# Optimization experiments

Measured on AMD Instinct MI355X. Metric: run time of the kernel, lower is better.

Reference implementation:

```python
import jax, jax.numpy as jnp
import numpy as np

DIM = 256      # d_model (MCMoE default dim=256)
E = 4          # experts: [CoAFusion, SNNFusion, DAMISLFusion, DropX2Fusion]
K = 2          # max_experts (top-k in cosine gate)
ATT = 128      # gated-attention hidden dim in DAMISL MIL pooling
N1, N2, B = 16384, 4096, 1


def setup_inputs() -> dict:
    key = jax.random.key(0)
    ks = jax.random.split(key, 16)
    s = 1.0 / np.sqrt(DIM)
    f32 = jnp.float32
    lin = lambda k, shape, scale: jax.random.normal(k, shape, f32) * scale
    return {
        'x1': jax.random.normal(ks[0], (B, N1, DIM), f32),
        'x2': jax.random.normal(ks[1], (B, N2, DIM), f32),
        # MM_CosineGate params: per-expert prototype rows + activation thresholds
        'sim_matrix': lin(ks[2], (E, DIM), 1.0),
        'gates': jnp.zeros((E,), f32),
        # SNNFusion: RMSNorm scales + two SNN blocks (Linear+ELU)
        'g1': jnp.ones((DIM,), f32),
        'g2': jnp.ones((DIM,), f32),
        'snn_w1': lin(ks[3], (DIM, DIM), s), 'snn_b1': jnp.zeros((DIM,), f32),
        'snn_w2': lin(ks[4], (DIM, DIM), s), 'snn_b2': jnp.zeros((DIM,), f32),
        # CoAFusion: single-head cross attention x1 -> x2
        'wq': lin(ks[5], (DIM, DIM), s), 'wk': lin(ks[6], (DIM, DIM), s),
        'wv': lin(ks[7], (DIM, DIM), s), 'wo': lin(ks[8], (DIM, DIM), s),
        # DAMISLFusion: gated-attention MIL pooling over x2 + fuse linear
        'va': lin(ks[9], (DIM, ATT), s), 'ua': lin(ks[10], (DIM, ATT), s),
        'wa': lin(ks[11], (ATT, 1), 1.0 / np.sqrt(ATT)),
        'wf': lin(ks[12], (DIM, DIM), s),
    }


def _rms(x, g):
    return x * jax.lax.rsqrt(jnp.mean(x * x, axis=-1, keepdims=True) + 1e-6) * g


def _forward(x1, x2, sim_matrix, gates, g1, g2, snn_w1, snn_b1, snn_w2, snn_b2,
             wq, wk, wv, wo, va, ua, wa, wf):
    # ---- MM_CosineGate: cosine similarity of pooled multimodal feature vs prototypes
    f = 0.5 * (x1.mean(axis=1) + x2.mean(axis=1))                       # [B, D]
    fn = f * jax.lax.rsqrt(jnp.sum(f * f, -1, keepdims=True) + 1e-8)
    sn = sim_matrix * jax.lax.rsqrt(jnp.sum(sim_matrix * sim_matrix, -1, keepdims=True) + 1e-8)
    scores = fn @ sn.T                                                  # [B, E]
    topv = jax.lax.top_k(scores, K)[0]                                  # [B, K]
    keep = (scores >= topv[:, -1:]) & (scores > gates[None, :])         # top-k AND above gate
    logits = jnp.where(keep, scores, 0.0)                               # [B, E], 0 for inactive

    # ---- Expert 0: CoAFusion (cross attention, residual)
    attn = jax.nn.softmax(
        jnp.einsum('bnd,bmd->bnm', x1 @ wq, x2 @ wk) / np.sqrt(DIM), axis=-1)  # [B, N1, N2]
    e0 = x1 + jnp.einsum('bnm,bmd->bnd', attn, x2 @ wv) @ wo

    # ---- Expert 1: SNNFusion (per-token SNN on x1 + pooled SNN on x2)
    e1 = jax.nn.elu(_rms(x1, g1) @ snn_w1 + snn_b1) \
         + jax.nn.elu(_rms(x2, g2) @ snn_w2 + snn_b2).mean(axis=1, keepdims=True)

    # ---- Expert 2: DAMISLFusion (gated-attention MIL pool of x2, broadcast fuse)
    h = jnp.tanh(x2 @ va) * jax.nn.sigmoid(x2 @ ua)                     # [B, N2, ATT]
    a = jax.nn.softmax((h @ wa)[..., 0], axis=1)                        # [B, N2]
    pooled = jnp.einsum('bm,bmd->bd', a, x2)                            # [B, D]
    e2 = x1 + (pooled @ wf)[:, None, :]

    # ---- Expert 3: DropX2Fusion (identity on x1)
    e3 = x1

    # ---- Weighted combine over selected experts (weight 0 => expert contributes 0),
    # then divide by number of selected experts (matches `outputs /= num_selected`).
    w = logits
    out = (w[:, 0, None, None] * e0 + w[:, 1, None, None] * e1
           + w[:, 2, None, None] * e2 + w[:, 3, None, None] * e3)
    num_sel = jnp.maximum(jnp.sum(logits > 0, axis=-1), 1).astype(out.dtype)  # [B]
    return out / num_sel[:, None, None]


def reference(x1, x2, sim_matrix, gates, g1, g2, snn_w1, snn_b1, snn_w2, snn_b2,
              wq, wk, wv, wo, va, ua, wa, wf):
    return _forward(x1, x2, sim_matrix, gates, g1, g2, snn_w1, snn_b1,
                    snn_w2, snn_b2, wq, wk, wv, wo, va, ua, wa, wf)
```

## Files before the change

kernel.cpp:

```cpp
#include <hip/hip_runtime.h>
#include <math.h>

#define N1 16384
#define N2 4096
#define DIM 256
#define ATT 128

typedef unsigned int uint32;
typedef __attribute__((ext_vector_type(4))) short s4v;
typedef __attribute__((ext_vector_type(8))) short s8v;
typedef __attribute__((ext_vector_type(16))) float f16v;
typedef __attribute__((ext_vector_type(2))) uint32 u2v;
typedef __attribute__((ext_vector_type(4))) uint32 u4v;

union S8U { s8v v; s4v h[2]; };

#define AS1C const __attribute__((address_space(1)))
#define AS3 __attribute__((address_space(3)))

#define WS_KPK 0
#define WS_VPK 524288
#define WS_WQT 1048576
#define WS_WOT 1081344
#define WS_W1T 1114112
#define WS_WKT 1146880
#define WS_WVT 1179648
#define WS_W2T 1212416
#define WS_VAT 1245184
#define WS_UAT 1261568
#define WS_ACC 1277952
#define WS_COLSUM1 (WS_ACC)
#define WS_COLSUM2 (WS_ACC+256)
#define WS_S2SUM  (WS_ACC+512)
#define WS_POOLED (WS_ACC+768)
#define WS_ALOGIT (WS_ACC+1024)
#define WS_AW     (WS_ALOGIT+4096)
#define WS_CVEC   (WS_AW+4096)
#define WS_GATE   (WS_CVEC+256)

#define L_K    0
#define L_V    65536
#define L_P    131072
#define L_LP   147456
#define L_LINV 149504
#define L_RRS  149760
#define L_RR   150016
#define L_X1PK  0
#define L_QPAD  65536
#define L_OBUF  0
#define L_X1PK2 65536
#define SMEM_BYTES 150272

__device__ __forceinline__ uint32 f2bf1(float f) {
    uint32 u = __float_as_uint(f);
    return (u + 0x7fffu + ((u >> 16) & 1u)) >> 16;
}
__device__ __forceinline__ uint32 f2bf2(float lo, float hi) {
    return f2bf1(lo) | (f2bf1(hi) << 16);
}
#define MFMA32(a, b, c) __builtin_amdgcn_mfma_f32_32x32x16_bf16((a), (b), (c), 0, 0, 0)

__global__ __launch_bounds__(256) void k_colsum12(const float* __restrict__ x1,
                                                  const float* __restrict__ x2,
                                                  float* __restrict__ ws)
{
    const int t = threadIdx.x;
    const int b = blockIdx.x;
    const float* src = (b < 256) ? x1 : x2;
    const int rbase = ((b < 256) ? b : (b - 256)) * 64;
    const int dsti = (b < 256) ? (WS_COLSUM1 + t) : (WS_COLSUM2 + t);
    float acc = 0.f;
    for (int r = 0; r < 64; ++r) acc += src[(size_t)(rbase + r) * DIM + t];
    atomicAdd(&ws[dsti], acc);
}

__global__ __launch_bounds__(256) void k_wpack(const float* __restrict__ wq,
    const float* __restrict__ wo, const float* __restrict__ snn_w1,
    const float* __restrict__ wk, const float* __restrict__ wv,
    const float* __restrict__ snn_w2,
    const float* __restrict__ va, const float* __restrict__ ua,
    const float* __restrict__ g1, const float* __restrict__ g2,
    float* __restrict__ ws)
{
    const int b = blockIdx.x;
    const int t = threadIdx.x;
    int mat, chunk, ncols;
    if (b < 192) { mat = b >> 5; chunk = b & 31; ncols = 256; }
    else { mat = 6 + ((b - 192) >> 4); chunk = (b - 192) & 15; ncols = 128; }
    const float* W;
    int dstoff;
    switch (mat) {
        case 0: W = wq;     dstoff = WS_WQT; break;
        case 1: W = wo;     dstoff = WS_WOT; break;
        case 2: W = snn_w1; dstoff = WS_W1T; break;
        case 3: W = wk;     dstoff = WS_WKT; break;
        case 4: W = wv;     dstoff = WS_WVT; break;
        case 5: W = snn_w2; dstoff = WS_W2T; break;
        case 6: W = va;     dstoff = WS_VAT; break;
        default: W = ua;    dstoff = WS_UAT; break;
    }
    unsigned short* dst = (unsigned short*)(ws + dstoff);
    const int e0 = chunk * 2048 + t * 8;
    const int k = (ncols == 256) ? (e0 >> 8) : (e0 >> 7);
    const int n0 = (ncols == 256) ? (e0 & 255) : (e0 & 127);
    const float4 v0 = *(const float4*)(W + k * ncols + n0);
    const float4 v1 = *(const float4*)(W + k * ncols + n0 + 4);
    const float sc = (mat == 2) ? g1[k] : ((mat == 5) ? g2[k] : 1.0f);
    float vals[8] = {v0.x, v0.y, v0.z, v0.w, v1.x, v1.y, v1.z, v1.w};
    const unsigned int sbase = (unsigned int)(k >> 4) * 512u + 32u * ((k >> 3) & 1) * 8u + (k & 7);
    #pragma unroll
    for (int jj = 0; jj < 8; ++jj) {
        const int n = n0 + jj;
        unsigned int off = (unsigned int)(n >> 5) * 16u * 512u + sbase + (unsigned int)(n & 31) * 8u;
        dst[off] = (unsigned short)f2bf1(vals[jj] * sc);
    }
}

__global__ __launch_bounds__(512) void k_x2prep2(const float* __restrict__ x2,
    const float* __restrict__ b2, const float* __restrict__ wa,
    float* __restrict__ ws)
{
    __shared__ char xps[16384];
    __shared__ float rrs[32];
    __shared__ float dlp[4][32];
    const int t = threadIdx.x;
    const int w = t >> 6;
    const int lane = t & 63;
    const int l31 = lane & 31;
    const int lh = lane >> 5;
    const int b = blockIdx.x;
    const int tb = b * 32;
    unsigned short* kpk = (unsigned short*)(ws + WS_KPK);
    unsigned short* vpk = (unsigned short*)(ws + WS_VPK);
    const char* wsb = (const char*)ws;
    const char* wkt = wsb + (size_t)WS_WKT * 4;
    const char* wvt = wsb + (size_t)WS_WVT * 4;
    const char* w2t = wsb + (size_t)WS_W2T * 4;
    const char* vat = wsb + (size_t)WS_VAT * 4;
    const char* uat = wsb + (size_t)WS_UAT * 4;

    #pragma unroll
    for (int i = 0; i < 2; ++i) {
        const int c = t + 512 * i;
        const int tk = c >> 5, d0 = (c & 31) * 8;
        const float4 a = *(const float4*)(x2 + (size_t)(tb + tk) * DIM + d0);
        const float4 bb = *(const float4*)(x2 + (size_t)(tb + tk) * DIM + d0 + 4);
        float ss = a.x*a.x + a.y*a.y + a.z*a.z + a.w*a.w
                 + bb.x*bb.x + bb.y*bb.y + bb.z*bb.z + bb.w*bb.w;
        #pragma unroll
        for (int o = 16; o > 0; o >>= 1) ss += __shfl_down(ss, o, 32);
        if ((t & 31) == 0) rrs[tk] = ss;
        u4v pk;
        pk.x = f2bf2(a.x, a.y); pk.y = f2bf2(a.z, a.w);
        pk.z = f2bf2(bb.x, bb.y); pk.w = f2bf2(bb.z, bb.w);
        *(u4v*)(xps + (d0 >> 4) * 1024 + (tk + 32 * ((d0 >> 3) & 1)) * 16) = pk;
    }
    __syncthreads();

    {
        f16v kacc = (f16v)0.0f;
        #pragma unroll
        for (int s = 0; s < 16; ++s) {
            const s8v a = *(const s8v*)(wkt + (w * 16 + s) * 1024 + lane * 16);
            const s8v bb = *(const s8v*)(xps + s * 1024 + lane * 16);
            kacc = MFMA32(a, bb, kacc);
        }
        #pragma unroll
        for (int g = 0; g < 4; ++g) {
            const unsigned int chunkK = (unsigned int)((b >> 1) * 32 + 2 * (2 * w + (g >> 1)) + (b & 1));
            const unsigned int off = chunkK * 512u + (unsigned int)(l31 + 32 * (g & 1)) * 8u + 4u * lh;
            u2v pk;
            pk.x = f2bf2(kacc[4 * g + 0], kacc[4 * g + 1]);
            pk.y = f2bf2(kacc[4 * g + 2], kacc[4 * g + 3]);
            *(u2v*)(kpk + off) = pk;
        }
    }
    {
        f16v vacc = (f16v)0.0f;
        #pragma unroll
        for (int s = 0; s < 16; ++s) {
            const s8v a = *(const s8v*)(xps + s * 1024 + lane * 16);
            const s8v bb = *(const s8v*)(wvt + (w * 16 + s) * 1024 + lane * 16);
            vacc = MFMA32(a, bb, vacc);
        }
        #pragma unroll
        for (int g = 0; g < 4; ++g) {
            const unsigned int chunkV = (unsigned int)((b >> 1) * 32 + 4 * w + 2 * (b & 1) + (g >> 1));
            const unsigned int off = chunkV * 512u + (unsigned int)(l31 + 32 * (g & 1)) * 8u + 4u * lh;
            u2v pk;
            pk.x = f2bf2(vacc[4 * g + 0], vacc[4 * g + 1]);
            pk.y = f2bf2(vacc[4 * g + 2], vacc[4 * g + 3]);
            *(u2v*)(vpk + off) = pk;
        }
    }
    {
        f16v sacc = (f16v)0.0f;
        #pragma unroll
        for (int s = 0; s < 16; ++s) {
            const s8v a = *(const s8v*)(w2t + (w * 16 + s) * 1024 + lane * 16);
            const s8v bb = *(const s8v*)(xps + s * 1024 + lane * 16);
            sacc = MFMA32(a, bb, sacc);
        }
        const float rrl = rsqrtf(rrs[l31] * (1.0f / DIM) + 1e-6f);
        #pragma unroll
        for (int g = 0; g < 4; ++g) {
            const float4 bb = *(const float4*)(b2 + 32 * w + 8 * g + 4 * lh);
            #pragma unroll
            for (int jj = 0; jj < 4; ++jj) {
                float v = sacc[4 * g + jj] * rrl + ((const float*)&bb)[jj];
                v = (v > 0.f) ? v : expm1f(v);
                v += __shfl_xor(v, 16); v += __shfl_xor(v, 8);
                v += __shfl_xor(v, 4);  v += __shfl_xor(v, 2);
                v += __shfl_xor(v, 1);
                if (l31 == 0) atomicAdd(&ws[WS_S2SUM + 32 * w + 8 * g + 4 * lh + jj], v);
            }
        }
    }
    if (w < 4) {
        f16v hv = (f16v)0.0f, hu = (f16v)0.0f;
        #pragma unroll
        for (int s = 0; s < 16; ++s) {
            const s8v bb = *(const s8v*)(xps + s * 1024 + lane * 16);
            const s8v a1 = *(const s8v*)(vat + (w * 16 + s) * 1024 + lane * 16);
            const s8v a2 = *(const s8v*)(uat + (w * 16 + s) * 1024 + lane * 16);
            hv = MFMA32(a1, bb, hv);
            hu = MFMA32(a2, bb, hu);
        }
        float acc = 0.f;
        #pragma unroll
        for (int g = 0; g < 4; ++g) {
            const float4 w4 = *(const float4*)(wa + 32 * w + 8 * g + 4 * lh);
            #pragma unroll
            for (int jj = 0; jj < 4; ++jj) {
                acc += tanhf(hv[4 * g + jj]) * (1.0f / (1.0f + expf(-hu[4 * g + jj])))
                       * ((const float*)&w4)[jj];
            }
        }
        acc += __shfl_xor(acc, 32);
        if (lh == 0) dlp[w][l31] = acc;
    }
    __syncthreads();
    if (t < 32) ws[WS_ALOGIT + tb + t] = dlp[0][t] + dlp[1][t] + dlp[2][t] + dlp[3][t];
}

__device__ __forceinline__ float block_sum256(float v, float* red, int t)
{
    red[t] = v; __syncthreads();
    for (int s = 128; s > 0; s >>= 1) { if (t < s) red[t] += red[t + s]; __syncthreads(); }
    const float r = red[0]; __syncthreads(); return r;
}
__device__ __forceinline__ float block_max256(float v, float* red, int t)
{
    red[t] = v; __syncthreads();
    for (int s = 128; s > 0; s >>= 1) { if (t < s) red[t] = fmaxf(red[t], red[t + s]); __syncthreads(); }
    const float r = red[0]; __syncthreads(); return r;
}

__global__ __launch_bounds__(256) void k_gate(const float* __restrict__ sim,
    const float* __restrict__ gates, float* __restrict__ ws)
{
    __shared__ float red[256];
    __shared__ float sc[4];
    const int t = threadIdx.x;
    const float f = 0.5f * (ws[WS_COLSUM1 + t] * (1.0f / N1) +
                            ws[WS_COLSUM2 + t] * (1.0f / N2));
    const float fs = block_sum256(f * f, red, t);
    const float rsqf = rsqrtf(fs + 1e-8f);
    for (int e = 0; e < 4; ++e) {
        const float sv = sim[e * DIM + t];
        const float n2 = block_sum256(sv * sv, red, t);
        const float dt = block_sum256(sv * f, red, t);
        if (t == 0) sc[e] = dt * rsqf * rsqrtf(n2 + 1e-8f);
    }
    __syncthreads();
    if (t == 0) {
        float a = -1e30f, b = -1e30f;
        #pragma unroll
        for (int e = 0; e < 4; ++e) {
            const float v = sc[e];
            if (v > a) { b = a; a = v; } else if (v > b) { b = v; }
        }
        float w[4]; int ns = 0;
        #pragma unroll
        for (int e = 0; e < 4; ++e) {
            const bool keep = (sc[e] >= b) && (sc[e] > gates[e]);
            w[e] = keep ? sc[e] : 0.f;
            if (w[e] > 0.f) ns++;
        }
        if (ns < 1) ns = 1;
        ws[WS_GATE + 0] = w[0]; ws[WS_GATE + 1] = w[1];
        ws[WS_GATE + 2] = w[2]; ws[WS_GATE + 3] = w[3];
        ws[WS_GATE + 4] = 1.0f / (float)ns;
        ws[WS_GATE + 5] = w[0] + w[2] + w[3];
    }
    __syncthreads();
    float mx = -1e30f;
    for (int i = t; i < N2; i += 256) mx = fmaxf(mx, ws[WS_ALOGIT + i]);
    mx = block_max256(mx, red, t);
    float sm = 0.f;
    for (int i = t; i < N2; i += 256) {
        const float e_ = expf(ws[WS_ALOGIT + i] - mx);
        ws[WS_AW + i] = e_;
        sm += e_;
    }
    sm = block_sum256(sm, red, t);
    const float is = 1.0f / sm;
    for (int i = t; i < N2; i += 256) ws[WS_AW + i] *= is;
}

__global__ __launch_bounds__(256) void k_pooled(const float* __restrict__ x2,
                                                float* __restrict__ ws)
{
    const int t = threadIdx.x;
    const int rbase = blockIdx.x * 64;
    float acc = 0.f;
    for (int r = 0; r < 64; ++r)
        acc = fmaf(ws[WS_AW + rbase + r], x2[(size_t)(rbase + r) * DIM + t], acc);
    atomicAdd(&ws[WS_POOLED + t], acc);
}

__global__ __launch_bounds__(256) void k_cvec(const float* __restrict__ wf,
                                              float* __restrict__ ws)
{
    __shared__ float pl[256];
    const int t = threadIdx.x;
    pl[t] = ws[WS_POOLED + t];
    __syncthreads();
    float acc = 0.f;
    for (int k = 0; k < 256; ++k) acc = fmaf(pl[k], wf[k * DIM + t], acc);
    const float w1 = ws[WS_GATE + 1], w2 = ws[WS_GATE + 2];
    ws[WS_CVEC + t] = w1 * (ws[WS_S2SUM + t] * (1.0f / N2)) + w2 * acc;
}

__global__ __launch_bounds__(512, 2) void k_flash(
    const float* __restrict__ x1, const float* __restrict__ b1,
    const float* __restrict__ wsf, float* __restrict__ out)
{
    extern __shared__ char sm[];
    const int t = threadIdx.x;
    const int w = t >> 6;
    const int lane = t & 63;
    const int l31 = lane & 31;
    const int lh = lane >> 5;
    const int qb = blockIdx.x * 64;
    const int kh = w >> 1, qh = w & 1;
    const int qp = w & 1, dpair = w >> 1;
    const char* wsb = (const char*)wsf;
    const char* kpk = wsb + (size_t)WS_KPK * 4;
    const char* vpk = wsb + (size_t)WS_VPK * 4;
    const char* wqt = wsb + (size_t)WS_WQT * 4;
    const char* wot = wsb + (size_t)WS_WOT * 4;
    const char* w1t = wsb + (size_t)WS_W1T * 4;

    auto stage64 = [&](const char* gbase, int ldsoff) {
        #pragma unroll
        for (int i = 0; i < 8; ++i) {
            const int c = w * 8 + i;
            __builtin_amdgcn_global_load_lds(
                (AS1C uint32*)(gbase + c * 1024 + lane * 16),
                (AS3 uint32*)(sm + ldsoff + c * 1024), 16, 0, 0);
        }
    };

    #pragma unroll
    for (int i = 0; i < 4; ++i) {
        const int c = t + 512 * i;
        const int q = c >> 5, d0 = (c & 31) * 8;
        const float4 a = *(const float4*)(x1 + (size_t)(qb + q) * DIM + d0);
        const float4 b = *(const float4*)(x1 + (size_t)(qb + q) * DIM + d0 + 4);
        float ss = a.x*a.x + a.y*a.y + a.z*a.z + a.w*a.w
                 + b.x*b.x + b.y*b.y + b.z*b.z + b.w*b.w;
        #pragma unroll
        for (int o = 16; o > 0; o >>= 1) ss += __shfl_down(ss, o, 32);
        if ((t & 31) == 0) *(float*)(sm + L_RRS + q * 4) = ss;
        u4v pk;
        pk.x = f2bf2(a.x, a.y); pk.y = f2bf2(a.z, a.w);
        pk.z = f2bf2(b.x, b.y); pk.w = f2bf2(b.z, b.w);
        *(u4v*)(sm + L_X1PK + ((q >> 5) * 16 + (d0 >> 4)) * 1024
                + ((q & 31) + 32 * ((d0 >> 3) & 1)) * 16) = pk;
    }
    __syncthreads();
    if (t < 64) {
        const float s2 = *(const float*)(sm + L_RRS + t * 4);
        *(float*)(sm + L_RR + t * 4) = rsqrtf(s2 * (1.0f / DIM) + 1e-6f);
    }
    #pragma unroll
    for (int i = 0; i < 2; ++i) {
        const int mt = w, qt = i;
        f16v qa = (f16v)0.0f;
        #pragma unroll
        for (int s = 0; s < 16; ++s) {
            const s8v a  = *(const s8v*)(wqt + (mt * 16 + s) * 1024 + lane * 16);
            const s8v bb = *(const s8v*)(sm + L_X1PK + (qt * 16 + s) * 1024 + lane * 16);
            qa = MFMA32(a, bb, qa);
        }
        const int q = qt * 32 + l31;
        #pragma unroll
        for (int g = 0; g < 4; ++g) {
            const int d0 = 32 * mt + 8 * g + 4 * lh;
            u2v pk;
            pk.x = f2bf2(qa[4 * g + 0], qa[4 * g + 1]);
            pk.y = f2bf2(qa[4 * g + 2], qa[4 * g + 3]);
            *(u2v*)(sm + L_QPAD + q * 520 + d0 * 2) = pk;
        }
    }
    __syncthreads();
    s8v qf[16];
    {
        const char* qbase = sm + L_QPAD + (qh * 32 + l31) * 520 + lh * 16;
        #pragma unroll
        for (int s = 0; s < 16; ++s) {
            S8U u;
            u.h[0] = *(const s4v*)(qbase + s * 32);
            u.h[1] = *(const s4v*)(qbase + s * 32 + 8);
            qf[s] = u.v;
        }
    }
    stage64(kpk, L_K);
    __syncthreads();

    f16v oacc0a = (f16v)0.0f, oacc0b = (f16v)0.0f;
    f16v oacc1a = (f16v)0.0f, oacc1b = (f16v)0.0f;
    float lsum = 0.0f;

    for (int tile = 0; tile < 32; ++tile) {
        stage64(vpk + (size_t)tile * 65536, L_V);
        f16v sacc0 = (f16v)0.0f, sacc1 = (f16v)0.0f;
        #pragma unroll
        for (int s2 = 0; s2 < 8; ++s2) {
            const s8v a0 = *(const s8v*)(sm + L_K
                + ((kh >> 1) * 32 + 2 * (2 * s2) + (kh & 1)) * 1024 + lane * 16);
            const s8v a1 = *(const s8v*)(sm + L_K
                + ((kh >> 1) * 32 + 2 * (2 * s2 + 1) + (kh & 1)) * 1024 + lane * 16);
            sacc0 = MFMA32(a0, qf[2 * s2], sacc0);
            sacc1 = MFMA32(a1, qf[2 * s2 + 1], sacc1);
        }
        #pragma unroll
        for (int g = 0; g < 4; ++g) {
            const float p0 = __expf((sacc0[4 * g + 0] + sacc1[4 * g + 0]) * 0.0625f);
            const float p1 = __expf((sacc0[4 * g + 1] + sacc1[4 * g + 1]) * 0.0625f);
            const float p2 = __expf((sacc0[4 * g + 2] + sacc1[4 * g + 2]) * 0.0625f);
            const float p3 = __expf((sacc0[4 * g + 3] + sacc1[4 * g + 3]) * 0.0625f);
            lsum += (p0 + p1) + (p2 + p3);
            const int keyo = 32 * kh + 8 * g + 4 * lh;
            const int kc = keyo >> 4, ko = keyo & 15;
            u2v pk; pk.x = f2bf2(p0, p1); pk.y = f2bf2(p2, p3);
            *(u2v*)(sm + L_P + (qh * 8 + kc) * 1024
                    + (l31 + 32 * (ko >> 3)) * 16 + (ko & 7) * 2) = pk;
        }
        __syncthreads();
        if (tile < 31) stage64(kpk + (size_t)(tile + 1) * 65536, L_K);
        s8v pf[8];
        #pragma unroll
        for (int kc = 0; kc < 8; ++kc)
            pf[kc] = *(const s8v*)(sm + L_P + (qp * 8 + kc) * 1024 + lane * 16);
        #pragma unroll
        for (int kc = 0; kc < 4; ++kc) {
            const int sub = 0, k3 = kc;
            const s8v a0 = *(const s8v*)(sm + L_V + (sub + 4 * (2 * dpair) + k3) * 1024 + lane * 16);
            const s8v a1 = *(const s8v*)(sm + L_V + (sub + 4 * (2 * dpair + 1) + k3) * 1024 + lane * 16);
            oacc0a = MFMA32(a0, pf[kc], oacc0a);
            oacc1a = MFMA32(a1, pf[kc], oacc1a);
        }
        #pragma unroll
        for (int kc = 4; kc < 8; ++kc) {
            const int sub = 32, k3 = kc & 3;
            const s8v a0 = *(const s8v*)(sm + L_V + (sub + 4 * (2 * dpair) + k3) * 1024 + lane * 16);
            const s8v a1 = *(const s8v*)(sm + L_V + (sub + 4 * (2 * dpair + 1) + k3) * 1024 + lane * 16);
            oacc0b = MFMA32(a0, pf[kc], oacc0b);
            oacc1b = MFMA32(a1, pf[kc], oacc1b);
        }
        __syncthreads();
    }

    *(float*)(sm + L_LP + ((w * 2 + lh) * 32 + l31) * 4) = lsum;
    __syncthreads();
    if (t < 64) {
        const int qh_ = t >> 5, c = t & 31;
        const float* lp = (const float*)(sm + L_LP);
        float l = 0.f;
        #pragma unroll
        for (int k2 = 0; k2 < 4; ++k2)
            l += lp[((k2 * 2 + qh_) * 2 + 0) * 32 + c]
               + lp[((k2 * 2 + qh_) * 2 + 1) * 32 + c];
        *(float*)(sm + L_LINV + t * 4) = 1.0f / l;
    }
    __syncthreads();
    {
        const float li = *(const float*)(sm + L_LINV + (qp * 32 + l31) * 4);
        #pragma unroll
        for (int half = 0; half < 2; ++half) {
            const f16v accA = half ? oacc1a : oacc0a;
            const f16v accB = half ? oacc1b : oacc0b;
            const int dc = 2 * dpair + half;
            #pragma unroll
            for (int g = 0; g < 4; ++g) {
                const int d0 = dc * 32 + 8 * g + 4 * lh;
                u2v pk;
                pk.x = f2bf2((accA[4 * g + 0] + accB[4 * g + 0]) * li,
                             (accA[4 * g + 1] + accB[4 * g + 1]) * li);
                pk.y = f2bf2((accA[4 * g + 2] + accB[4 * g + 2]) * li,
                             (accA[4 * g + 3] + accB[4 * g + 3]) * li);
                *(u2v*)(sm + L_OBUF + (qp * 16 + (d0 >> 4)) * 1024
                        + (l31 + 32 * ((d0 >> 3) & 1)) * 16 + (d0 & 7) * 2) = pk;
            }
        }
    }
    #pragma unroll
    for (int i = 0; i < 4; ++i) {
        const int c = t + 512 * i;
        const int q = c >> 5, d0 = (c & 31) * 8;
        const float4 a = *(const float4*)(x1 + (size_t)(qb + q) * DIM + d0);
        const float4 b = *(const float4*)(x1 + (size_t)(qb + q) * DIM + d0 + 4);
        u4v pk;
        pk.x = f2bf2(a.x, a.y); pk.y = f2bf2(a.z, a.w);
        pk.z = f2bf2(b.x, b.y); pk.w = f2bf2(b.z, b.w);
        *(u4v*)(sm + L_X1PK2 + ((q >> 5) * 16 + (d0 >> 4)) * 1024
                + ((q & 31) + 32 * ((d0 >> 3) & 1)) * 16) = pk;
    }
    __syncthreads();
    const float gw0 = wsf[WS_GATE + 0], gw1 = wsf[WS_GATE + 1];
    const float ginv = wsf[WS_GATE + 4], gcx1 = wsf[WS_GATE + 5];
    #pragma unroll
    for (int i = 0; i < 2; ++i) {
        const int mt = w, qt = i;
        f16v ea = (f16v)0.0f, sa = (f16v)0.0f;
        for (int s = 0; s < 16; ++s) {
            const s8v awo = *(const s8v*)(wot + (mt * 16 + s) * 1024 + lane * 16);
            const s8v aw1 = *(const s8v*)(w1t + (mt * 16 + s) * 1024 + lane * 16);
            const s8v bo = *(const s8v*)(sm + L_OBUF + (qt * 16 + s) * 1024 + lane * 16);
            const s8v bx = *(const s8v*)(sm + L_X1PK2 + (qt * 16 + s) * 1024 + lane * 16);
            ea = MFMA32(awo, bo, ea);
            sa = MFMA32(aw1, bx, sa);
        }
        const int q = qt * 32 + l31;
        const float rrq = *(const float*)(sm + L_RR + q * 4);
        #pragma unroll
        for (int g = 0; g < 4; ++g) {
            const int d0 = 32 * mt + 8 * g + 4 * lh;
            const float4 cv = *(const float4*)(wsf + WS_CVEC + d0);
            const float4 bb = *(const float4*)(b1 + d0);
            const float4 xx = *(const float4*)(x1 + (size_t)(qb + q) * DIM + d0);
            float ev0 = sa[4 * g + 0] * rrq + bb.x; ev0 = (ev0 > 0.f) ? ev0 : expm1f(ev0);
            float ev1 = sa[4 * g + 1] * rrq + bb.y; ev1 = (ev1 > 0.f) ? ev1 : expm1f(ev1);
            float ev2 = sa[4 * g + 2] * rrq + bb.z; ev2 = (ev2 > 0.f) ? ev2 : expm1f(ev2);
            float ev3 = sa[4 * g + 3] * rrq + bb.w; ev3 = (ev3 > 0.f) ? ev3 : expm1f(ev3);
            float4 o;
            o.x = ginv * (gcx1 * xx.x + gw0 * ea[4 * g + 0] + gw1 * ev0 + cv.x);
            o.y = ginv * (gcx1 * xx.y + gw0 * ea[4 * g + 1] + gw1 * ev1 + cv.y);
            o.z = ginv * (gcx1 * xx.z + gw0 * ea[4 * g + 2] + gw1 * ev2 + cv.z);
            o.w = ginv * (gcx1 * xx.w + gw0 * ea[4 * g + 3] + gw1 * ev3 + cv.w);
            *(float4*)(out + (size_t)(qb + q) * DIM + d0) = o;
        }
    }
}

extern "C" void kernel_launch(void* const* d_in, const int* in_sizes, int n_in,
                              void* d_out, int out_size, void* d_ws, size_t ws_size,
                              hipStream_t stream)
{
    (void)in_sizes; (void)n_in; (void)out_size; (void)ws_size;
    const float* x1    = (const float*)d_in[0];
    const float* x2    = (const float*)d_in[1];
    const float* sim   = (const float*)d_in[2];
    const float* gates = (const float*)d_in[3];
    const float* g1    = (const float*)d_in[4];
    const float* g2    = (const float*)d_in[5];
    const float* w1m   = (const float*)d_in[6];
    const float* b1    = (const float*)d_in[7];
    const float* w2m   = (const float*)d_in[8];
    const float* b2    = (const float*)d_in[9];
    const float* wq    = (const float*)d_in[10];
    const float* wk    = (const float*)d_in[11];
    const float* wv    = (const float*)d_in[12];
    const float* wo    = (const float*)d_in[13];
    const float* va    = (const float*)d_in[14];
    const float* ua    = (const float*)d_in[15];
    const float* wa    = (const float*)d_in[16];
    const float* wf    = (const float*)d_in[17];
    float* ws  = (float*)d_ws;
    float* out = (float*)d_out;

    hipMemsetAsync(ws + WS_ACC, 0, 1024 * sizeof(float), stream);
    hipLaunchKernelGGL(k_colsum12, dim3(320), dim3(256), 0, stream, x1, x2, ws);
    hipLaunchKernelGGL(k_wpack, dim3(224), dim3(256), 0, stream,
                       wq, wo, w1m, wk, wv, w2m, va, ua, g1, g2, ws);
    hipLaunchKernelGGL(k_x2prep2, dim3(N2 / 32), dim3(512), 0, stream, x2, b2, wa, ws);
    hipLaunchKernelGGL(k_gate, dim3(1), dim3(256), 0, stream, sim, gates, ws);
    hipLaunchKernelGGL(k_pooled, dim3(N2 / 64), dim3(256), 0, stream, x2, ws);
    hipLaunchKernelGGL(k_cvec, dim3(1), dim3(256), 0, stream, wf, ws);
    hipLaunchKernelGGL(k_flash, dim3(N1 / 64), dim3(512), SMEM_BYTES, stream,
                       x1, b1, ws, out);
}
```

Baseline: 278.3 us.

## Fuse all stages into one cooperative persistent kernel with grid syncs

```diff
diff --git a/kernel.cpp b/kernel.cpp
--- a/kernel.cpp
+++ b/kernel.cpp
@@ -1,5 +1,8 @@
 #include <hip/hip_runtime.h>
+#include <hip/hip_cooperative_groups.h>
 #include <math.h>
+
+namespace cg = cooperative_groups;
 
 #define N1 16384
 #define N2 4096
@@ -60,497 +63,504 @@
 }
 #define MFMA32(a, b, c) __builtin_amdgcn_mfma_f32_32x32x16_bf16((a), (b), (c), 0, 0, 0)
 
-__global__ __launch_bounds__(256) void k_colsum12(const float* __restrict__ x1,
-                                                  const float* __restrict__ x2,
-                                                  float* __restrict__ ws)
+__global__ __launch_bounds__(512, 2) void k_all(
+    const float* __restrict__ x1, const float* __restrict__ x2,
+    const float* __restrict__ sim, const float* __restrict__ gates,
+    const float* __restrict__ g1, const float* __restrict__ g2,
+    const float* __restrict__ snn_w1, const float* __restrict__ b1,
+    const float* __restrict__ snn_w2, const float* __restrict__ b2,
+    const float* __restrict__ wq, const float* __restrict__ wk,
+    const float* __restrict__ wv, const float* __restrict__ wo,
+    const float* __restrict__ va, const float* __restrict__ ua,
+    const float* __restrict__ wa, const float* __restrict__ wf,
+    float* __restrict__ ws, float* __restrict__ out)
 {
+    extern __shared__ char sm[];
+    cg::grid_group grid = cg::this_grid();
     const int t = threadIdx.x;
     const int b = blockIdx.x;
-    const float* src = (b < 256) ? x1 : x2;
-    const int rbase = ((b < 256) ? b : (b - 256)) * 64;
-    const int dsti = (b < 256) ? (WS_COLSUM1 + t) : (WS_COLSUM2 + t);
-    float acc = 0.f;
-    for (int r = 0; r < 64; ++r) acc += src[(size_t)(rbase + r) * DIM + t];
-    atomicAdd(&ws[dsti], acc);
-}
-
-__global__ __launch_bounds__(256) void k_wpack(const float* __restrict__ wq,
-    const float* __restrict__ wo, const float* __restrict__ snn_w1,
-    const float* __restrict__ wk, const float* __restrict__ wv,
-    const float* __restrict__ snn_w2,
-    const float* __restrict__ va, const float* __restrict__ ua,
-    const float* __restrict__ g1, const float* __restrict__ g2,
-    float* __restrict__ ws)
-{
-    const int b = blockIdx.x;
-    const int t = threadIdx.x;
-    int mat, chunk, ncols;
-    if (b < 192) { mat = b >> 5; chunk = b & 31; ncols = 256; }
-    else { mat = 6 + ((b - 192) >> 4); chunk = (b - 192) & 15; ncols = 128; }
-    const float* W;
-    int dstoff;
-    switch (mat) {
-        case 0: W = wq;     dstoff = WS_WQT; break;
-        case 1: W = wo;     dstoff = WS_WOT; break;
-        case 2: W = snn_w1; dstoff = WS_W1T; break;
-        case 3: W = wk;     dstoff = WS_WKT; break;
-        case 4: W = wv;     dstoff = WS_WVT; break;
-        case 5: W = snn_w2; dstoff = WS_W2T; break;
-        case 6: W = va;     dstoff = WS_VAT; break;
-        default: W = ua;    dstoff = WS_UAT; break;
-    }
-    unsigned short* dst = (unsigned short*)(ws + dstoff);
-    const int e0 = chunk * 2048 + t * 8;
-    const int k = (ncols == 256) ? (e0 >> 8) : (e0 >> 7);
-    const int n0 = (ncols == 256) ? (e0 & 255) : (e0 & 127);
-    const float4 v0 = *(const float4*)(W + k * ncols + n0);
-    const float4 v1 = *(const float4*)(W + k * ncols + n0 + 4);
-    const float sc = (mat == 2) ? g1[k] : ((mat == 5) ? g2[k] : 1.0f);
-    float vals[8] = {v0.x, v0.y, v0.z, v0.w, v1.x, v1.y, v1.z, v1.w};
-    const unsigned int sbase = (unsigned int)(k >> 4) * 512u + 32u * ((k >> 3) & 1) * 8u + (k & 7);
-    #pragma unroll
-    for (int jj = 0; jj < 8; ++jj) {
-        const int n = n0 + jj;
-        unsigned int off = (unsigned int)(n >> 5) * 16u * 512u + sbase + (unsigned int)(n & 31) * 8u;
-        dst[off] = (unsigned short)f2bf1(vals[jj] * sc);
-    }
-}
-
-__global__ __launch_bounds__(512) void k_x2prep2(const float* __restrict__ x2,
-    const float* __restrict__ b2, const float* __restrict__ wa,
-    float* __restrict__ ws)
-{
-    __shared__ char xps[16384];
-    __shared__ float rrs[32];
-    __shared__ float dlp[4][32];
-    const int t = threadIdx.x;
     const int w = t >> 6;
     const int lane = t & 63;
     const int l31 = lane & 31;
     const int lh = lane >> 5;
-    const int b = blockIdx.x;
-    const int tb = b * 32;
-    unsigned short* kpk = (unsigned short*)(ws + WS_KPK);
-    unsigned short* vpk = (unsigned short*)(ws + WS_VPK);
-    const char* wsb = (const char*)ws;
-    const char* wkt = wsb + (size_t)WS_WKT * 4;
-    const char* wvt = wsb + (size_t)WS_WVT * 4;
-    const char* w2t = wsb + (size_t)WS_W2T * 4;
-    const char* vat = wsb + (size_t)WS_VAT * 4;
-    const char* uat = wsb + (size_t)WS_UAT * 4;
-
-    #pragma unroll
-    for (int i = 0; i < 2; ++i) {
-        const int c = t + 512 * i;
-        const int tk = c >> 5, d0 = (c & 31) * 8;
-        const float4 a = *(const float4*)(x2 + (size_t)(tb + tk) * DIM + d0);
-        const float4 bb = *(const float4*)(x2 + (size_t)(tb + tk) * DIM + d0 + 4);
-        float ss = a.x*a.x + a.y*a.y + a.z*a.z + a.w*a.w
-                 + bb.x*bb.x + bb.y*bb.y + bb.z*bb.z + bb.w*bb.w;
+
+    if (b == 0) {
+        for (int i = t; i < 1024; i += 512) ws[WS_ACC + i] = 0.f;
+    }
+    __threadfence();
+    grid.sync();
+
+    if (t < 256) {
+        if (b < 224) {
+            int mat, chunk, ncols;
+            if (b < 192) { mat = b >> 5; chunk = b & 31; ncols = 256; }
+            else { mat = 6 + ((b - 192) >> 4); chunk = (b - 192) & 15; ncols = 128; }
+            const float* W;
+            int dstoff;
+            switch (mat) {
+                case 0: W = wq;     dstoff = WS_WQT; break;
+                case 1: W = wo;     dstoff = WS_WOT; break;
+                case 2: W = snn_w1; dstoff = WS_W1T; break;
+                case 3: W = wk;     dstoff = WS_WKT; break;
+                case 4: W = wv;     dstoff = WS_WVT; break;
+                case 5: W = snn_w2; dstoff = WS_W2T; break;
+                case 6: W = va;     dstoff = WS_VAT; break;
+                default: W = ua;    dstoff = WS_UAT; break;
+            }
+            unsigned short* dst = (unsigned short*)(ws + dstoff);
+            const int e0 = chunk * 2048 + t * 8;
+            const int k = (ncols == 256) ? (e0 >> 8) : (e0 >> 7);
+            const int n0 = (ncols == 256) ? (e0 & 255) : (e0 & 127);
+            const float4 v0 = *(const float4*)(W + k * ncols + n0);
+            const float4 v1 = *(const float4*)(W + k * ncols + n0 + 4);
+            const float sc = (mat == 2) ? g1[k] : ((mat == 5) ? g2[k] : 1.0f);
+            float vals[8] = {v0.x, v0.y, v0.z, v0.w, v1.x, v1.y, v1.z, v1.w};
+            const unsigned int sbase = (unsigned int)(k >> 4) * 512u
+                + 32u * ((k >> 3) & 1) * 8u + (k & 7);
+            #pragma unroll
+            for (int jj = 0; jj < 8; ++jj) {
+                const int n = n0 + jj;
+                unsigned int off = (unsigned int)(n >> 5) * 16u * 512u + sbase
+                                 + (unsigned int)(n & 31) * 8u;
+                dst[off] = (unsigned short)f2bf1(vals[jj] * sc);
+            }
+        }
+    } else {
+        const int col = t - 256;
+        float acc = 0.f;
+        for (int r = 0; r < 64; ++r) acc += x1[(size_t)(b * 64 + r) * DIM + col];
+        atomicAdd(&ws[WS_COLSUM1 + col], acc);
+        if (b < 64) {
+            float a2 = 0.f;
+            for (int r = 0; r < 64; ++r) a2 += x2[(size_t)(b * 64 + r) * DIM + col];
+            atomicAdd(&ws[WS_COLSUM2 + col], a2);
+        }
+    }
+    __threadfence();
+    grid.sync();
+
+    if (b < 128) {
+        char* xps = sm;
+        float* rrs = (float*)(sm + 16384);
+        float* dlp = (float*)(sm + 16512);
+        const int tb = b * 32;
+        unsigned short* kpk = (unsigned short*)(ws + WS_KPK);
+        unsigned short* vpk = (unsigned short*)(ws + WS_VPK);
+        const char* wsb = (const char*)ws;
+        const char* wkt = wsb + (size_t)WS_WKT * 4;
+        const char* wvt = wsb + (size_t)WS_WVT * 4;
+        const char* w2t = wsb + (size_t)WS_W2T * 4;
+        const char* vat = wsb + (size_t)WS_VAT * 4;
+        const char* uat = wsb + (size_t)WS_UAT * 4;
+
         #pragma unroll
-        for (int o = 16; o > 0; o >>= 1) ss += __shfl_down(ss, o, 32);
-        if ((t & 31) == 0) rrs[tk] = ss;
-        u4v pk;
-        pk.x = f2bf2(a.x, a.y); pk.y = f2bf2(a.z, a.w);
-        pk.z = f2bf2(bb.x, bb.y); pk.w = f2bf2(bb.z, bb.w);
-        *(u4v*)(xps + (d0 >> 4) * 1024 + (tk + 32 * ((d0 >> 3) & 1)) * 16) = pk;
+        for (int i = 0; i < 2; ++i) {
+            const int c = t + 512 * i;
+            const int tk = c >> 5, d0 = (c & 31) * 8;
+            const float4 a = *(const float4*)(x2 + (size_t)(tb + tk) * DIM + d0);
+            const float4 bb = *(const float4*)(x2 + (size_t)(tb + tk) * DIM + d0 + 4);
+            float ss = a.x*a.x + a.y*a.y + a.z*a.z + a.w*a.w
+                     + bb.x*bb.x + bb.y*bb.y + bb.z*bb.z + bb.w*bb.w;
+            #pragma unroll
+            for (int o = 16; o > 0; o >>= 1) ss += __shfl_down(ss, o, 32);
+            if ((t & 31) == 0) rrs[tk] = ss;
+            u4v pk;
+            pk.x = f2bf2(a.x, a.y); pk.y = f2bf2(a.z, a.w);
+            pk.z = f2bf2(bb.x, bb.y); pk.w = f2bf2(bb.z, bb.w);
+            *(u4v*)(xps + (d0 >> 4) * 1024 + (tk + 32 * ((d0 >> 3) & 1)) * 16) = pk;
+        }
+        __syncthreads();
+
+        {
+            f16v kacc = (f16v)0.0f;
+            #pragma unroll
+            for (int s = 0; s < 16; ++s) {
+                const s8v a = *(const s8v*)(wkt + (w * 16 + s) * 1024 + lane * 16);
+                const s8v bb = *(const s8v*)(xps + s * 1024 + lane * 16);
+                kacc = MFMA32(a, bb, kacc);
+            }
+            #pragma unroll
+            for (int g = 0; g < 4; ++g) {
+                const unsigned int chunkK =
+                    (unsigned int)((b >> 1) * 32 + 2 * (2 * w + (g >> 1)) + (b & 1));
+                const unsigned int off = chunkK * 512u
+                    + (unsigned int)(l31 + 32 * (g & 1)) * 8u + 4u * lh;
+                u2v pk;
+                pk.x = f2bf2(kacc[4 * g + 0], kacc[4 * g + 1]);
+                pk.y = f2bf2(kacc[4 * g + 2], kacc[4 * g + 3]);
+                *(u2v*)(kpk + off) = pk;
+            }
+        }
+        {
+            f16v vacc = (f16v)0.0f;
+            #pragma unroll
+            for (int s = 0; s < 16; ++s) {
+                const s8v a = *(const s8v*)(xps + s * 1024 + lane * 16);
+                const s8v bb = *(const s8v*)(wvt + (w * 16 + s) * 1024 + lane * 16);
+                vacc = MFMA32(a, bb, vacc);
+            }
+            #pragma unroll
+            for (int g = 0; g < 4; ++g) {
+                const unsigned int chunkV =
+                    (unsigned int)((b >> 1) * 32 + 4 * w + 2 * (b & 1) + (g >> 1));
+                const unsigned int off = chunkV * 512u
+                    + (unsigned int)(l31 + 32 * (g & 1)) * 8u + 4u * lh;
+                u2v pk;
+                pk.x = f2bf2(vacc[4 * g + 0], vacc[4 * g + 1]);
+                pk.y = f2bf2(vacc[4 * g + 2], vacc[4 * g + 3]);
+                *(u2v*)(vpk + off) = pk;
+            }
+        }
+        {
+            f16v sacc = (f16v)0.0f;
+            #pragma unroll
+            for (int s = 0; s < 16; ++s) {
+                const s8v a = *(const s8v*)(w2t + (w * 16 + s) * 1024 + lane * 16);
+                const s8v bb = *(const s8v*)(xps + s * 1024 + lane * 16);
+                sacc = MFMA32(a, bb, sacc);
+            }
+            const float rrl = rsqrtf(rrs[l31] * (1.0f / DIM) + 1e-6f);
+            #pragma unroll
+            for (int g = 0; g < 4; ++g) {
+                const float4 bb = *(const float4*)(b2 + 32 * w + 8 * g + 4 * lh);
+                #pragma unroll
+                for (int jj = 0; jj < 4; ++jj) {
+                    float v = sacc[4 * g + jj] * rrl + ((const float*)&bb)[jj];
+                    v = (v > 0.f) ? v : expm1f(v);
+                    v += __shfl_xor(v, 16); v += __shfl_xor(v, 8);
+                    v += __shfl_xor(v, 4);  v += __shfl_xor(v, 2);
+                    v += __shfl_xor(v, 1);
+                    if (l31 == 0)
+                        atomicAdd(&ws[WS_S2SUM + 32 * w + 8 * g + 4 * lh + jj], v);
+                }
+            }
+        }
+        if (w < 4) {
+            f16v hv = (f16v)0.0f, hu = (f16v)0.0f;
+            #pragma unroll
+            for (int s = 0; s < 16; ++s) {
+                const s8v bb = *(const s8v*)(xps + s * 1024 + lane * 16);
+                const s8v a1 = *(const s8v*)(vat + (w * 16 + s) * 1024 + lane * 16);
+                const s8v a2 = *(const s8v*)(uat + (w * 16 + s) * 1024 + lane * 16);
+                hv = MFMA32(a1, bb, hv);
+                hu = MFMA32(a2, bb, hu);
+            }
+            float acc = 0.f;
+            #pragma unroll
+            for (int g = 0; g < 4; ++g) {
+                const float4 w4 = *(const float4*)(wa + 32 * w + 8 * g + 4 * lh);
+                #pragma unroll
+                for (int jj = 0; jj < 4; ++jj) {
+                    acc += tanhf(hv[4 * g + jj])
+                         * (1.0f / (1.0f + expf(-hu[4 * g + jj])))
+                         * ((const float*)&w4)[jj];
+                }
+            }
+            acc += __shfl_xor(acc, 32);
+            if (lh == 0) dlp[w * 32 + l31] = acc;
+        }
+        __syncthreads();
+        if (t < 32)
+            ws[WS_ALOGIT + tb + t] = dlp[t] + dlp[32 + t] + dlp[64 + t] + dlp[96 + t];
     }
-    __syncthreads();
-
-    {
-        f16v kacc = (f16v)0.0f;
-        #pragma unroll
-        for (int s = 0; s < 16; ++s) {
-            const s8v a = *(const s8v*)(wkt + (w * 16 + s) * 1024 + lane * 16);
-            const s8v bb = *(const s8v*)(xps + s * 1024 + lane * 16);
-            kacc = MFMA32(a, bb, kacc);
-        }
-        #pragma unroll
-        for (int g = 0; g < 4; ++g) {
-            const unsigned int chunkK = (unsigned int)((b >> 1) * 32 + 2 * (2 * w + (g >> 1)) + (b & 1));
-            const unsigned int off = chunkK * 512u + (unsigned int)(l31 + 32 * (g & 1)) * 8u + 4u * lh;
-            u2v pk;
-            pk.x = f2bf2(kacc[4 * g + 0], kacc[4 * g + 1]);
-            pk.y = f2bf2(kacc[4 * g + 2], kacc[4 * g + 3]);
-            *(u2v*)(kpk + off) = pk;
-        }
-    }
-    {
-        f16v vacc = (f16v)0.0f;
-        #pragma unroll
-        for (int s = 0; s < 16; ++s) {
-            const s8v a = *(const s8v*)(xps + s * 1024 + lane * 16);
-            const s8v bb = *(const s8v*)(wvt + (w * 16 + s) * 1024 + lane * 16);
-            vacc = MFMA32(a, bb, vacc);
-        }
-        #pragma unroll
-        for (int g = 0; g < 4; ++g) {
-            const unsigned int chunkV = (unsigned int)((b >> 1) * 32 + 4 * w + 2 * (b & 1) + (g >> 1));
-            const unsigned int off = chunkV * 512u + (unsigned int)(l31 + 32 * (g & 1)) * 8u + 4u * lh;
-            u2v pk;
-            pk.x = f2bf2(vacc[4 * g + 0], vacc[4 * g + 1]);
-            pk.y = f2bf2(vacc[4 * g + 2], vacc[4 * g + 3]);
-            *(u2v*)(vpk + off) = pk;
-        }
-    }
-    {
-        f16v sacc = (f16v)0.0f;
-        #pragma unroll
-        for (int s = 0; s < 16; ++s) {
-            const s8v a = *(const s8v*)(w2t + (w * 16 + s) * 1024 + lane * 16);
-            const s8v bb = *(const s8v*)(xps + s * 1024 + lane * 16);
-            sacc = MFMA32(a, bb, sacc);
-        }
-        const float rrl = rsqrtf(rrs[l31] * (1.0f / DIM) + 1e-6f);
-        #pragma unroll
-        for (int g = 0; g < 4; ++g) {
-            const float4 bb = *(const float4*)(b2 + 32 * w + 8 * g + 4 * lh);
-            #pragma unroll
-            for (int jj = 0; jj < 4; ++jj) {
-                float v = sacc[4 * g + jj] * rrl + ((const float*)&bb)[jj];
-                v = (v > 0.f) ? v : expm1f(v);
-                v += __shfl_xor(v, 16); v += __shfl_xor(v, 8);
-                v += __shfl_xor(v, 4);  v += __shfl_xor(v, 2);
-                v += __shfl_xor(v, 1);
-                if (l31 == 0) atomicAdd(&ws[WS_S2SUM + 32 * w + 8 * g + 4 * lh + jj], v);
-            }
-        }
-    }
-    if (w < 4) {
-        f16v hv = (f16v)0.0f, hu = (f16v)0.0f;
-        #pragma unroll
-        for (int s = 0; s < 16; ++s) {
-            const s8v bb = *(const s8v*)(xps + s * 1024 + lane * 16);
-            const s8v a1 = *(const s8v*)(vat + (w * 16 + s) * 1024 + lane * 16);
-            const s8v a2 = *(const s8v*)(uat + (w * 16 + s) * 1024 + lane * 16);
-            hv = MFMA32(a1, bb, hv);
-            hu = MFMA32(a2, bb, hu);
-        }
-        float acc = 0.f;
-        #pragma unroll
-        for (int g = 0; g < 4; ++g) {
-            const float4 w4 = *(const float4*)(wa + 32 * w + 8 * g + 4 * lh);
-            #pragma unroll
-            for (int jj = 0; jj < 4; ++jj) {
-                acc += tanhf(hv[4 * g + jj]) * (1.0f / (1.0f + expf(-hu[4 * g + jj])))
-                       * ((const float*)&w4)[jj];
-            }
-        }
-        acc += __shfl_xor(acc, 32);
-        if (lh == 0) dlp[w][l31] = acc;
-    }
-    __syncthreads();
-    if (t < 32) ws[WS_ALOGIT + tb + t] = dlp[0][t] + dlp[1][t] + dlp[2][t] + dlp[3][t];
-}
-
-__device__ __forceinline__ float block_sum256(float v, float* red, int t)
-{
-    red[t] = v; __syncthreads();
-    for (int s = 128; s > 0; s >>= 1) { if (t < s) red[t] += red[t + s]; __syncthreads(); }
-    const float r = red[0]; __syncthreads(); return r;
-}
-__device__ __forceinline__ float block_max256(float v, float* red, int t)
-{
-    red[t] = v; __syncthreads();
-    for (int s = 128; s > 0; s >>= 1) { if (t < s) red[t] = fmaxf(red[t], red[t + s]); __syncthreads(); }
-    const float r = red[0]; __syncthreads(); return r;
-}
-
-__global__ __launch_bounds__(256) void k_gate(const float* __restrict__ sim,
-    const float* __restrict__ gates, float* __restrict__ ws)
-{
-    __shared__ float red[256];
-    __shared__ float sc[4];
-    const int t = threadIdx.x;
-    const float f = 0.5f * (ws[WS_COLSUM1 + t] * (1.0f / N1) +
-                            ws[WS_COLSUM2 + t] * (1.0f / N2));
-    const float fs = block_sum256(f * f, red, t);
-    const float rsqf = rsqrtf(fs + 1e-8f);
-    for (int e = 0; e < 4; ++e) {
-        const float sv = sim[e * DIM + t];
-        const float n2 = block_sum256(sv * sv, red, t);
-        const float dt = block_sum256(sv * f, red, t);
-        if (t == 0) sc[e] = dt * rsqf * rsqrtf(n2 + 1e-8f);
-    }
-    __syncthreads();
-    if (t == 0) {
-        float a = -1e30f, b = -1e30f;
+    __threadfence();
+    grid.sync();
+
+    if (b == 0) {
+        float* red  = (float*)sm;
+        float* acc9 = (float*)(sm + 2048);
+        if (t < 9) acc9[t] = 0.f;
+        __syncthreads();
+        float fv = 0.f;
+        if (t < 256)
+            fv = 0.5f * (ws[WS_COLSUM1 + t] * (1.0f / N1)
+                       + ws[WS_COLSUM2 + t] * (1.0f / N2));
+        {
+            float p = fv * fv;
+            #pragma unroll
+            for (int o = 32; o > 0; o >>= 1) p += __shfl_xor(p, o);
+            if (lane == 0) atomicAdd(&acc9[0], p);
+        }
         #pragma unroll
         for (int e = 0; e < 4; ++e) {
-            const float v = sc[e];
-            if (v > a) { b = a; a = v; } else if (v > b) { b = v; }
-        }
-        float w[4]; int ns = 0;
+            const float sv = (t < 256) ? sim[e * DIM + t] : 0.f;
+            float pn = sv * sv, pd = sv * fv;
+            #pragma unroll
+            for (int o = 32; o > 0; o >>= 1) { pn += __shfl_xor(pn, o); pd += __shfl_xor(pd, o); }
+            if (lane == 0) { atomicAdd(&acc9[1 + e], pn); atomicAdd(&acc9[5 + e], pd); }
+        }
+        __syncthreads();
+        if (t == 0) {
+            const float rsqf = rsqrtf(acc9[0] + 1e-8f);
+            float sc[4];
+            #pragma unroll
+            for (int e = 0; e < 4; ++e)
+                sc[e] = acc9[5 + e] * rsqf * rsqrtf(acc9[1 + e] + 1e-8f);
+            float a = -1e30f, bb = -1e30f;
+            #pragma unroll
+            for (int e = 0; e < 4; ++e) {
+                const float v = sc[e];
+                if (v > a) { bb = a; a = v; } else if (v > bb) { bb = v; }
+            }
+            float wv_[4]; int ns = 0;
+            #pragma unroll
+            for (int e = 0; e < 4; ++e) {
+                const bool keep = (sc[e] >= bb) && (sc[e] > gates[e]);
+                wv_[e] = keep ? sc[e] : 0.f;
+                if (wv_[e] > 0.f) ns++;
+            }
+            if (ns < 1) ns = 1;
+            ws[WS_GATE + 0] = wv_[0]; ws[WS_GATE + 1] = wv_[1];
+            ws[WS_GATE + 2] = wv_[2]; ws[WS_GATE + 3] = wv_[3];
+            ws[WS_GATE + 4] = 1.0f / (float)ns;
+            ws[WS_GATE + 5] = wv_[0] + wv_[2] + wv_[3];
+        }
+        float mx = -1e30f;
+        for (int i = t; i < N2; i += 512) mx = fmaxf(mx, ws[WS_ALOGIT + i]);
+        red[t] = mx; __syncthreads();
+        for (int s = 256; s > 0; s >>= 1) {
+            if (t < s) red[t] = fmaxf(red[t], red[t + s]);
+            __syncthreads();
+        }
+        mx = red[0]; __syncthreads();
+        float sum = 0.f;
+        for (int i = t; i < N2; i += 512) {
+            const float e_ = __expf(ws[WS_ALOGIT + i] - mx);
+            ws[WS_AW + i] = e_;
+            sum += e_;
+        }
+        red[t] = sum; __syncthreads();
+        for (int s = 256; s > 0; s >>= 1) {
+            if (t < s) red[t] += red[t + s];
+            __syncthreads();
+        }
+        const float is = 1.0f / red[0];
+        for (int i = t; i < N2; i += 512) ws[WS_AW + i] *= is;
+    }
+    __threadfence();
+    grid.sync();
+
+    if (b < 128) {
+        const int col = t & 255, rh = t >> 8;
+        const int r0 = b * 32 + rh * 16;
+        float acc = 0.f;
+        for (int r = 0; r < 16; ++r)
+            acc = fmaf(ws[WS_AW + r0 + r], x2[(size_t)(r0 + r) * DIM + col], acc);
+        atomicAdd(&ws[WS_POOLED + col], acc);
+    }
+    __threadfence();
+    grid.sync();
+
+    if (b == 0) {
+        float* pl = (float*)sm;
+        if (t < 256) pl[t] = ws[WS_POOLED + t];
+        __syncthreads();
+        if (t < 256) {
+            float acc = 0.f;
+            for (int k = 0; k < 256; ++k) acc = fmaf(pl[k], wf[k * DIM + t], acc);
+            ws[WS_CVEC + t] = ws[WS_GATE + 1] * (ws[WS_S2SUM + t] * (1.0f / N2))
+                            + ws[WS_GATE + 2] * acc;
+        }
+    }
+    __threadfence();
+    grid.sync();
+
+    {
+        const int qb = b * 64;
+        const int kh = w >> 1, qh = w & 1;
+        const int qp = w & 1, dpair = w >> 1;
+        const char* wsb = (const char*)ws;
+        const char* kpk = wsb + (size_t)WS_KPK * 4;
+        const char* vpk = wsb + (size_t)WS_VPK * 4;
+        const char* wqt = wsb + (size_t)WS_WQT * 4;
+        const char* wot = wsb + (size_t)WS_WOT * 4;
+        const char* w1t = wsb + (size_t)WS_W1T * 4;
+
+        auto stage64 = [&](const char* gbase, int ldsoff) {
+            #pragma unroll
+            for (int i = 0; i < 8; ++i) {
+                const int c = w * 8 + i;
+                __builtin_amdgcn_global_load_lds(
+                    (AS1C uint32*)(gbase + c * 1024 + lane * 16),
+                    (AS3 uint32*)(sm + ldsoff + c * 1024), 16, 0, 0);
+            }
+        };
+
         #pragma unroll
-        for (int e = 0; e < 4; ++e) {
-            const bool keep = (sc[e] >= b) && (sc[e] > gates[e]);
-            w[e] = keep ? sc[e] : 0.f;
-            if (w[e] > 0.f) ns++;
-        }
-        if (ns < 1) ns = 1;
-        ws[WS_GATE + 0] = w[0]; ws[WS_GATE + 1] = w[1];
-        ws[WS_GATE + 2] = w[2]; ws[WS_GATE + 3] = w[3];
-        ws[WS_GATE + 4] = 1.0f / (float)ns;
-        ws[WS_GATE + 5] = w[0] + w[2] + w[3];
-    }
-    __syncthreads();
-    float mx = -1e30f;
-    for (int i = t; i < N2; i += 256) mx = fmaxf(mx, ws[WS_ALOGIT + i]);
-    mx = block_max256(mx, red, t);
-    float sm = 0.f;
-    for (int i = t; i < N2; i += 256) {
-        const float e_ = expf(ws[WS_ALOGIT + i] - mx);
-        ws[WS_AW + i] = e_;
-        sm += e_;
-    }
-    sm = block_sum256(sm, red, t);
-    const float is = 1.0f / sm;
-    for (int i = t; i < N2; i += 256) ws[WS_AW + i] *= is;
-}
-
-__global__ __launch_bounds__(256) void k_pooled(const float* __restrict__ x2,
-                                                float* __restrict__ ws)
-{
-    const int t = threadIdx.x;
-    const int rbase = blockIdx.x * 64;
-    float acc = 0.f;
-    for (int r = 0; r < 64; ++r)
-        acc = fmaf(ws[WS_AW + rbase + r], x2[(size_t)(rbase + r) * DIM + t], acc);
-    atomicAdd(&ws[WS_POOLED + t], acc);
-}
-
-__global__ __launch_bounds__(256) void k_cvec(const float* __restrict__ wf,
-                                              float* __restrict__ ws)
-{
-    __shared__ float pl[256];
-    const int t = threadIdx.x;
-    pl[t] = ws[WS_POOLED + t];
-    __syncthreads();
-    float acc = 0.f;
-    for (int k = 0; k < 256; ++k) acc = fmaf(pl[k], wf[k * DIM + t], acc);
-    const float w1 = ws[WS_GATE + 1], w2 = ws[WS_GATE + 2];
-    ws[WS_CVEC + t] = w1 * (ws[WS_S2SUM + t] * (1.0f / N2)) + w2 * acc;
-}
-
-__global__ __launch_bounds__(512, 2) void k_flash(
-    const float* __restrict__ x1, const float* __restrict__ b1,
-    const float* __restrict__ wsf, float* __restrict__ out)
-{
-    extern __shared__ char sm[];
-    const int t = threadIdx.x;
-    const int w = t >> 6;
-    const int lane = t & 63;
-    const int l31 = lane & 31;
-    const int lh = lane >> 5;
-    const int qb = blockIdx.x * 64;
-    const int kh = w >> 1, qh = w & 1;
-    const int qp = w & 1, dpair = w >> 1;
-    const char* wsb = (const char*)wsf;
-    const char* kpk = wsb + (size_t)WS_KPK * 4;
-    const char* vpk = wsb + (size_t)WS_VPK * 4;
-    const char* wqt = wsb + (size_t)WS_WQT * 4;
-    const char* wot = wsb + (size_t)WS_WOT * 4;
-    const char* w1t = wsb + (size_t)WS_W1T * 4;
-
-    auto stage64 = [&](const char* gbase, int ldsoff) {
+        for (int i = 0; i < 4; ++i) {
+            const int c = t + 512 * i;
+            const int q = c >> 5, d0 = (c & 31) * 8;
+            const float4 a = *(const float4*)(x1 + (size_t)(qb + q) * DIM + d0);
+            const float4 bb = *(const float4*)(x1 + (size_t)(qb + q) * DIM + d0 + 4);
+            float ss = a.x*a.x + a.y*a.y + a.z*a.z + a.w*a.w
+                     + bb.x*bb.x + bb.y*bb.y + bb.z*bb.z + bb.w*bb.w;
+            #pragma unroll
+            for (int o = 16; o > 0; o >>= 1) ss += __shfl_down(ss, o, 32);
+            if ((t & 31) == 0) *(float*)(sm + L_RRS + q * 4) = ss;
+            u4v pk;
+            pk.x = f2bf2(a.x, a.y); pk.y = f2bf2(a.z, a.w);
+            pk.z = f2bf2(bb.x, bb.y); pk.w = f2bf2(bb.z, bb.w);
+            *(u4v*)(sm + L_X1PK + ((q >> 5) * 16 + (d0 >> 4)) * 1024
+                    + ((q & 31) + 32 * ((d0 >> 3) & 1)) * 16) = pk;
+        }
+        __syncthreads();
+        if (t < 64) {
+            const float s2 = *(const float*)(sm + L_RRS + t * 4);
+            *(float*)(sm + L_RR + t * 4) = rsqrtf(s2 * (1.0f / DIM) + 1e-6f);
+        }
         #pragma unroll
-        for (int i = 0; i < 8; ++i) {
-            const int c = w * 8 + i;
-            __builtin_amdgcn_global_load_lds(
-                (AS1C uint32*)(gbase + c * 1024 + lane * 16),
-                (AS3 uint32*)(sm + ldsoff + c * 1024), 16, 0, 0);
-        }
-    };
-
-    #pragma unroll
-    for (int i = 0; i < 4; ++i) {
-        const int c = t + 512 * i;
-        const int q = c >> 5, d0 = (c & 31) * 8;
-        const float4 a = *(const float4*)(x1 + (size_t)(qb + q) * DIM + d0);
-        const float4 b = *(const float4*)(x1 + (size_t)(qb + q) * DIM + d0 + 4);
-        float ss = a.x*a.x + a.y*a.y + a.z*a.z + a.w*a.w
-                 + b.x*b.x + b.y*b.y + b.z*b.z + b.w*b.w;
+        for (int i = 0; i < 2; ++i) {
+            const int mt = w, qt = i;
+            f16v qa = (f16v)0.0f;
+            #pragma unroll
+            for (int s = 0; s < 16; ++s) {
+                const s8v a  = *(const s8v*)(wqt + (mt * 16 + s) * 1024 + lane * 16);
+                const s8v bb = *(const s8v*)(sm + L_X1PK + (qt * 16 + s) * 1024 + lane * 16);
+                qa = MFMA32(a, bb, qa);
+            }
+            const int q = qt * 32 + l31;
+            #pragma unroll
+            for (int g = 0; g < 4; ++g) {
+                const int d0 = 32 * mt + 8 * g + 4 * lh;
+                u2v pk;
+                pk.x = f2bf2(qa[4 * g + 0], qa[4 * g + 1]);
+                pk.y = f2bf2(qa[4 * g + 2], qa[4 * g + 3]);
+                *(u2v*)(sm + L_QPAD + q * 520 + d0 * 2) = pk;
+            }
+        }
+        __syncthreads();
+        s8v qf[16];
+        {
+            const char* qbase = sm + L_QPAD + (qh * 32 + l31) * 520 + lh * 16;
+            #pragma unroll
+            for (int s = 0; s < 16; ++s) {
+                S8U u;
+                u.h[0] = *(const s4v*)(qbase + s * 32);
+                u.h[1] = *(const s4v*)(qbase + s * 32 + 8);
+                qf[s] = u.v;
+            }
+        }
+        stage64(kpk, L_K);
+        __syncthreads();
+
+        f16v oacc0 = (f16v)0.0f, oacc1 = (f16v)0.0f;
+        float lsum = 0.0f;
+
+        for (int tile = 0; tile < 32; ++tile) {
+            stage64(vpk + (size_t)tile * 65536, L_V);
+            f16v sacc = (f16v)0.0f;
+            #pragma unroll
+            for (int s = 0; s < 16; ++s) {
+                const s8v a = *(const s8v*)(sm + L_K
+                    + ((kh >> 1) * 32 + 2 * s + (kh & 1)) * 1024 + lane * 16);
+                sacc = MFMA32(a, qf[s], sacc);
+            }
+            #pragma unroll
+            for (int g = 0; g < 4; ++g) {
+                const float p0 = __expf(sacc[4 * g + 0] * 0.0625f);
+                const float p1 = __expf(sacc[4 * g + 1] * 0.0625f);
+                const float p2 = __expf(sacc[4 * g + 2] * 0.0625f);
+                const float p3 = __expf(sacc[4 * g + 3] * 0.0625f);
+                lsum += (p0 + p1) + (p2 + p3);
+                const int keyo = 32 * kh + 8 * g + 4 * lh;
+                const int kc = keyo >> 4, ko = keyo & 15;
+                u2v pk; pk.x = f2bf2(p0, p1); pk.y = f2bf2(p2, p3);
+                *(u2v*)(sm + L_P + (qh * 8 + kc) * 1024
+                        + (l31 + 32 * (ko >> 3)) * 16 + (ko & 7) * 2) = pk;
+            }
+            __syncthreads();
+            if (tile < 31) stage64(kpk + (size_t)(tile + 1) * 65536, L_K);
+            s8v pf[8];
+            #pragma unroll
+            for (int kc = 0; kc < 8; ++kc)
+                pf[kc] = *(const s8v*)(sm + L_P + (qp * 8 + kc) * 1024 + lane * 16);
+            #pragma unroll
+            for (int kc = 0; kc < 8; ++kc) {
+                const int sub = (kc >> 2) * 32, k3 = kc & 3;
+                const s8v a0 = *(const s8v*)(sm + L_V + (sub + 4 * (2 * dpair) + k3) * 1024 + lane * 16);
+                const s8v a1 = *(const s8v*)(sm + L_V + (sub + 4 * (2 * dpair + 1) + k3) * 1024 + lane * 16);
+                oacc0 = MFMA32(a0, pf[kc], oacc0);
+                oacc1 = MFMA32(a1, pf[kc], oacc1);
+            }
+            __syncthreads();
+        }
+
+        *(float*)(sm + L_LP + ((w * 2 + lh) * 32 + l31) * 4) = lsum;
+        __syncthreads();
+        if (t < 64) {
+            const int qh_ = t >> 5, c = t & 31;
+            const float* lp = (const float*)(sm + L_LP);
+            float l = 0.f;
+            #pragma unroll
+            for (int k2 = 0; k2 < 4; ++k2)
+                l += lp[((k2 * 2 + qh_) * 2 + 0) * 32 + c]
+                   + lp[((k2 * 2 + qh_) * 2 + 1) * 32 + c];
+            *(float*)(sm + L_LINV + t * 4) = 1.0f / l;
+        }
+        __syncthreads();
+        {
+            const float li = *(const float*)(sm + L_LINV + (qp * 32 + l31) * 4);
+            #pragma unroll
+            for (int half = 0; half < 2; ++half) {
+                const f16v acc = half ? oacc1 : oacc0;
+                const int dc = 2 * dpair + half;
+                #pragma unroll
+                for (int g = 0; g < 4; ++g) {
+                    const int d0 = dc * 32 + 8 * g + 4 * lh;
+                    u2v pk;
+                    pk.x = f2bf2(acc[4 * g + 0] * li, acc[4 * g + 1] * li);
+                    pk.y = f2bf2(acc[4 * g + 2] * li, acc[4 * g + 3] * li);
+                    *(u2v*)(sm + L_OBUF + (qp * 16 + (d0 >> 4)) * 1024
+                            + (l31 + 32 * ((d0 >> 3) & 1)) * 16 + (d0 & 7) * 2) = pk;
+                }
+            }
+        }
         #pragma unroll
-        for (int o = 16; o > 0; o >>= 1) ss += __shfl_down(ss, o, 32);
-        if ((t & 31) == 0) *(float*)(sm + L_RRS + q * 4) = ss;
-        u4v pk;
-        pk.x = f2bf2(a.x, a.y); pk.y = f2bf2(a.z, a.w);
-        pk.z = f2bf2(b.x, b.y); pk.w = f2bf2(b.z, b.w);
-        *(u4v*)(sm + L_X1PK + ((q >> 5) * 16 + (d0 >> 4)) * 1024
-                + ((q & 31) + 32 * ((d0 >> 3) & 1)) * 16) = pk;
-    }
-    __syncthreads();
-    if (t < 64) {
-        const float s2 = *(const float*)(sm + L_RRS + t * 4);
-        *(float*)(sm + L_RR + t * 4) = rsqrtf(s2 * (1.0f / DIM) + 1e-6f);
-    }
-    #pragma unroll
-    for (int i = 0; i < 2; ++i) {
-        const int mt = w, qt = i;
-        f16v qa = (f16v)0.0f;
+        for (int i = 0; i < 4; ++i) {
+            const int c = t + 512 * i;
+            const int q = c >> 5, d0 = (c & 31) * 8;
+            const float4 a = *(const float4*)(x1 + (size_t)(qb + q) * DIM + d0);
+            const float4 bb = *(const float4*)(x1 + (size_t)(qb + q) * DIM + d0 + 4);
+            u4v pk;
+            pk.x = f2bf2(a.x, a.y); pk.y = f2bf2(a.z, a.w);
+            pk.z = f2bf2(bb.x, bb.y); pk.w = f2bf2(bb.z, bb.w);
+            *(u4v*)(sm + L_X1PK2 + ((q >> 5) * 16 + (d0 >> 4)) * 1024
+                    + ((q & 31) + 32 * ((d0 >> 3) & 1)) * 16) = pk;
+        }
+        __syncthreads();
+        const float gw0 = ws[WS_GATE + 0], gw1 = ws[WS_GATE + 1];
+        const float ginv = ws[WS_GATE + 4], gcx1 = ws[WS_GATE + 5];
         #pragma unroll
-        for (int s = 0; s < 16; ++s) {
-            const s8v a  = *(const s8v*)(wqt + (mt * 16 + s) * 1024 + lane * 16);
-            const s8v bb = *(const s8v*)(sm + L_X1PK + (qt * 16 + s) * 1024 + lane * 16);
-            qa = MFMA32(a, bb, qa);
-        }
-        const int q = qt * 32 + l31;
-        #pragma unroll
-        for (int g = 0; g < 4; ++g) {
-            const int d0 = 32 * mt + 8 * g + 4 * lh;
-            u2v pk;
-            pk.x = f2bf2(qa[4 * g + 0], qa[4 * g + 1]);
-            pk.y = f2bf2(qa[4 * g + 2], qa[4 * g + 3]);
-            *(u2v*)(sm + L_QPAD + q * 520 + d0 * 2) = pk;
-        }
-    }
-    __syncthreads();
-    s8v qf[16];
-    {
-        const char* qbase = sm + L_QPAD + (qh * 32 + l31) * 520 + lh * 16;
-        #pragma unroll
-        for (int s = 0; s < 16; ++s) {
-            S8U u;
-            u.h[0] = *(const s4v*)(qbase + s * 32);
-            u.h[1] = *(const s4v*)(qbase + s * 32 + 8);
-            qf[s] = u.v;
-        }
-    }
-    stage64(kpk, L_K);
-    __syncthreads();
-
-    f16v oacc0a = (f16v)0.0f, oacc0b = (f16v)0.0f;
-    f16v oacc1a = (f16v)0.0f, oacc1b = (f16v)0.0f;
-    float lsum = 0.0f;
-
-    for (int tile = 0; tile < 32; ++tile) {
-        stage64(vpk + (size_t)tile * 65536, L_V);
-        f16v sacc0 = (f16v)0.0f, sacc1 = (f16v)0.0f;
-        #pragma unroll
-        for (int s2 = 0; s2 < 8; ++s2) {
-            const s8v a0 = *(const s8v*)(sm + L_K
-                + ((kh >> 1) * 32 + 2 * (2 * s2) + (kh & 1)) * 1024 + lane * 16);
-            const s8v a1 = *(const s8v*)(sm + L_K
-                + ((kh >> 1) * 32 + 2 * (2 * s2 + 1) + (kh & 1)) * 1024 + lane * 16);
-            sacc0 = MFMA32(a0, qf[2 * s2], sacc0);
-            sacc1 = MFMA32(a1, qf[2 * s2 + 1], sacc1);
-        }
-        #pragma unroll
-        for (int g = 0; g < 4; ++g) {
-            const float p0 = __expf((sacc0[4 * g + 0] + sacc1[4 * g + 0]) * 0.0625f);
-            const float p1 = __expf((sacc0[4 * g + 1] + sacc1[4 * g + 1]) * 0.0625f);
-            const float p2 = __expf((sacc0[4 * g + 2] + sacc1[4 * g + 2]) * 0.0625f);
-            const float p3 = __expf((sacc0[4 * g + 3] + sacc1[4 * g + 3]) * 0.0625f);
-            lsum += (p0 + p1) + (p2 + p3);
-            const int keyo = 32 * kh + 8 * g + 4 * lh;
-            const int kc = keyo >> 4, ko = keyo & 15;
-            u2v pk; pk.x = f2bf2(p0, p1); pk.y = f2bf2(p2, p3);
-            *(u2v*)(sm + L_P + (qh * 8 + kc) * 1024
-                    + (l31 + 32 * (ko >> 3)) * 16 + (ko & 7) * 2) = pk;
-        }
-        __syncthreads();
-        if (tile < 31) stage64(kpk + (size_t)(tile + 1) * 65536, L_K);
-        s8v pf[8];
-        #pragma unroll
-        for (int kc = 0; kc < 8; ++kc)
-            pf[kc] = *(const s8v*)(sm + L_P + (qp * 8 + kc) * 1024 + lane * 16);
-        #pragma unroll
-        for (int kc = 0; kc < 4; ++kc) {
-            const int sub = 0, k3 = kc;
-            const s8v a0 = *(const s8v*)(sm + L_V + (sub + 4 * (2 * dpair) + k3) * 1024 + lane * 16);
-            const s8v a1 = *(const s8v*)(sm + L_V + (sub + 4 * (2 * dpair + 1) + k3) * 1024 + lane * 16);
-            oacc0a = MFMA32(a0, pf[kc], oacc0a);
-            oacc1a = MFMA32(a1, pf[kc], oacc1a);
-        }
-        #pragma unroll
-        for (int kc = 4; kc < 8; ++kc) {
-            const int sub = 32, k3 = kc & 3;
-            const s8v a0 = *(const s8v*)(sm + L_V + (sub + 4 * (2 * dpair) + k3) * 1024 + lane * 16);
-            const s8v a1 = *(const s8v*)(sm + L_V + (sub + 4 * (2 * dpair + 1) + k3) * 1024 + lane * 16);
-            oacc0b = MFMA32(a0, pf[kc], oacc0b);
-            oacc1b = MFMA32(a1, pf[kc], oacc1b);
-        }
-        __syncthreads();
-    }
-
-    *(float*)(sm + L_LP + ((w * 2 + lh) * 32 + l31) * 4) = lsum;
-    __syncthreads();
-    if (t < 64) {
-        const int qh_ = t >> 5, c = t & 31;
-        const float* lp = (const float*)(sm + L_LP);
-        float l = 0.f;
-        #pragma unroll
-        for (int k2 = 0; k2 < 4; ++k2)
-            l += lp[((k2 * 2 + qh_) * 2 + 0) * 32 + c]
-               + lp[((k2 * 2 + qh_) * 2 + 1) * 32 + c];
-        *(float*)(sm + L_LINV + t * 4) = 1.0f / l;
-    }
-    __syncthreads();
-    {
-        const float li = *(const float*)(sm + L_LINV + (qp * 32 + l31) * 4);
-        #pragma unroll
-        for (int half = 0; half < 2; ++half) {
-            const f16v accA = half ? oacc1a : oacc0a;
-            const f16v accB = half ? oacc1b : oacc0b;
-            const int dc = 2 * dpair + half;
+        for (int i = 0; i < 2; ++i) {
+            const int mt = w, qt = i;
+            f16v ea = (f16v)0.0f, sa = (f16v)0.0f;
+            for (int s = 0; s < 16; ++s) {
+                const s8v awo = *(const s8v*)(wot + (mt * 16 + s) * 1024 + lane * 16);
+                const s8v aw1 = *(const s8v*)(w1t + (mt * 16 + s) * 1024 + lane * 16);
+                const s8v bo = *(const s8v*)(sm + L_OBUF + (qt * 16 + s) * 1024 + lane * 16);
+                const s8v bx = *(const s8v*)(sm + L_X1PK2 + (qt * 16 + s) * 1024 + lane * 16);
+                ea = MFMA32(awo, bo, ea);
+                sa = MFMA32(aw1, bx, sa);
+            }
+            const int q = qt * 32 + l31;
+            const float rrq = *(const float*)(sm + L_RR + q * 4);
             #pragma unroll
             for (int g = 0; g < 4; ++g) {
-                const int d0 = dc * 32 + 8 * g + 4 * lh;
-                u2v pk;
-                pk.x = f2bf2((accA[4 * g + 0] + accB[4 * g + 0]) * li,
-                             (accA[4 * g + 1] + accB[4 * g + 1]) * li);
-                pk.y = f2bf2((accA[4 * g + 2] + accB[4 * g + 2]) * li,
-                             (accA[4 * g + 3] + accB[4 * g + 3]) * li);
-                *(u2v*)(sm + L_OBUF + (qp * 16 + (d0 >> 4)) * 1024
-                        + (l31 + 32 * ((d0 >> 3) & 1)) * 16 + (d0 & 7) * 2) = pk;
-            }
-        }
-    }
-    #pragma unroll
-    for (int i = 0; i < 4; ++i) {
-        const int c = t + 512 * i;
-        const int q = c >> 5, d0 = (c & 31) * 8;
-        const float4 a = *(const float4*)(x1 + (size_t)(qb + q) * DIM + d0);
-        const float4 b = *(const float4*)(x1 + (size_t)(qb + q) * DIM + d0 + 4);
-        u4v pk;
-        pk.x = f2bf2(a.x, a.y); pk.y = f2bf2(a.z, a.w);
-        pk.z = f2bf2(b.x, b.y); pk.w = f2bf2(b.z, b.w);
-        *(u4v*)(sm + L_X1PK2 + ((q >> 5) * 16 + (d0 >> 4)) * 1024
-                + ((q & 31) + 32 * ((d0 >> 3) & 1)) * 16) = pk;
-    }
-    __syncthreads();
-    const float gw0 = wsf[WS_GATE + 0], gw1 = wsf[WS_GATE + 1];
-    const float ginv = wsf[WS_GATE + 4], gcx1 = wsf[WS_GATE + 5];
-    #pragma unroll
-    for (int i = 0; i < 2; ++i) {
-        const int mt = w, qt = i;
-        f16v ea = (f16v)0.0f, sa = (f16v)0.0f;
-        for (int s = 0; s < 16; ++s) {
-            const s8v awo = *(const s8v*)(wot + (mt * 16 + s) * 1024 + lane * 16);
-            const s8v aw1 = *(const s8v*)(w1t + (mt * 16 + s) * 1024 + lane * 16);
-            const s8v bo = *(const s8v*)(sm + L_OBUF + (qt * 16 + s) * 1024 + lane * 16);
-            const s8v bx = *(const s8v*)(sm + L_X1PK2 + (qt * 16 + s) * 1024 + lane * 16);
-            ea = MFMA32(awo, bo, ea);
-            sa = MFMA32(aw1, bx, sa);
-        }
-        const int q = qt * 32 + l31;
-        const float rrq = *(const float*)(sm + L_RR + q * 4);
-        #pragma unroll
-        for (int g = 0; g < 4; ++g) {
-            const int d0 = 32 * mt + 8 * g + 4 * lh;
-            const float4 cv = *(const float4*)(wsf + WS_CVEC + d0);
-            const float4 bb = *(const float4*)(b1 + d0);
-            const float4 xx = *(const float4*)(x1 + (size_t)(qb + q) * DIM + d0);
-            float ev0 = sa[4 * g + 0] * rrq + bb.x; ev0 = (ev0 > 0.f) ? ev0 : expm1f(ev0);
-            float ev1 = sa[4 * g + 1] * rrq + bb.y; ev1 = (ev1 > 0.f) ? ev1 : expm1f(ev1);
-            float ev2 = sa[4 * g + 2] * rrq + bb.z; ev2 = (ev2 > 0.f) ? ev2 : expm1f(ev2);
-            float ev3 = sa[4 * g + 3] * rrq + bb.w; ev3 = (ev3 > 0.f) ? ev3 : expm1f(ev3);
-            float4 o;
-            o.x = ginv * (gcx1 * xx.x + gw0 * ea[4 * g + 0] + gw1 * ev0 + cv.x);
-            o.y = ginv * (gcx1 * xx.y + gw0 * ea[4 * g + 1] + gw1 * ev1 + cv.y);
-            o.z = ginv * (gcx1 * xx.z + gw0 * ea[4 * g + 2] + gw1 * ev2 + cv.z);
-            o.w = ginv * (gcx1 * xx.w + gw0 * ea[4 * g + 3] + gw1 * ev3 + cv.w);
-            *(float4*)(out + (size_t)(qb + q) * DIM + d0) = o;
+                const int d0 = 32 * mt + 8 * g + 4 * lh;
+                const float4 cv = *(const float4*)(ws + WS_CVEC + d0);
+                const float4 bb = *(const float4*)(b1 + d0);
+                const float4 xx = *(const float4*)(x1 + (size_t)(qb + q) * DIM + d0);
+                float ev0 = sa[4 * g + 0] * rrq + bb.x; ev0 = (ev0 > 0.f) ? ev0 : expm1f(ev0);
+                float ev1 = sa[4 * g + 1] * rrq + bb.y; ev1 = (ev1 > 0.f) ? ev1 : expm1f(ev1);
+                float ev2 = sa[4 * g + 2] * rrq + bb.z; ev2 = (ev2 > 0.f) ? ev2 : expm1f(ev2);
+                float ev3 = sa[4 * g + 3] * rrq + bb.w; ev3 = (ev3 > 0.f) ? ev3 : expm1f(ev3);
+                float4 o;
+                o.x = ginv * (gcx1 * xx.x + gw0 * ea[4 * g + 0] + gw1 * ev0 + cv.x);
+                o.y = ginv * (gcx1 * xx.y + gw0 * ea[4 * g + 1] + gw1 * ev1 + cv.y);
+                o.z = ginv * (gcx1 * xx.z + gw0 * ea[4 * g + 2] + gw1 * ev2 + cv.z);
+                o.w = ginv * (gcx1 * xx.w + gw0 * ea[4 * g + 3] + gw1 * ev3 + cv.w);
+                *(float4*)(out + (size_t)(qb + q) * DIM + d0) = o;
+            }
         }
     }
 }
@@ -581,14 +591,13 @@
     float* ws  = (float*)d_ws;
     float* out = (float*)d_out;
 
-    hipMemsetAsync(ws + WS_ACC, 0, 1024 * sizeof(float), stream);
-    hipLaunchKernelGGL(k_colsum12, dim3(320), dim3(256), 0, stream, x1, x2, ws);
-    hipLaunchKernelGGL(k_wpack, dim3(224), dim3(256), 0, stream,
-                       wq, wo, w1m, wk, wv, w2m, va, ua, g1, g2, ws);
-    hipLaunchKernelGGL(k_x2prep2, dim3(N2 / 32), dim3(512), 0, stream, x2, b2, wa, ws);
-    hipLaunchKernelGGL(k_gate, dim3(1), dim3(256), 0, stream, sim, gates, ws);
-    hipLaunchKernelGGL(k_pooled, dim3(N2 / 64), dim3(256), 0, stream, x2, ws);
-    hipLaunchKernelGGL(k_cvec, dim3(1), dim3(256), 0, stream, wf, ws);
-    hipLaunchKernelGGL(k_flash, dim3(N1 / 64), dim3(512), SMEM_BYTES, stream,
-                       x1, b1, ws, out);
+    void* args[20] = {
+        (void*)&x1, (void*)&x2, (void*)&sim, (void*)&gates,
+        (void*)&g1, (void*)&g2, (void*)&w1m, (void*)&b1,
+        (void*)&w2m, (void*)&b2, (void*)&wq, (void*)&wk,
+        (void*)&wv, (void*)&wo, (void*)&va, (void*)&ua,
+        (void*)&wa, (void*)&wf, (void*)&ws, (void*)&out
+    };
+    hipLaunchCooperativeKernel((const void*)k_all, dim3(256), dim3(512),
+                               args, SMEM_BYTES, stream);
 }
```

Result: slower. 679.8 us (+144.2%).
